# Performance work log

Hardware: AMD Instinct MI355X
Metric: run time of the kernel (lower is better)

The kernel has to match this reference:

```python
import jax, jax.numpy as jnp
import numpy as np

B, T, N, D = 8, 12, 1024, 64
E, M, L = 64, 16, 2


def _ln(x, g, b, eps=1e-5):
    mu = x.mean(-1, keepdims=True)
    var = ((x - mu) ** 2).mean(-1, keepdims=True)
    return (x - mu) * jax.lax.rsqrt(var + eps) * g + b


def setup_inputs() -> dict:
    key = jax.random.key(0)
    ks = jax.random.split(key, 10)
    return {
        "H_temp": jax.random.normal(ks[0], (B, T, N, D), dtype=jnp.float32),
        "A_static": jax.random.uniform(ks[1], (N, N), dtype=jnp.float32),
        "W_Q": jax.random.normal(ks[2], (E, D)) / np.sqrt(D),
        "W_K": jax.random.normal(ks[3], (E, E)) / np.sqrt(E),
        "W_V": jax.random.normal(ks[4], (D, E)) / np.sqrt(E),
        "PHI_m": jax.random.normal(ks[5], (M, E)) / np.sqrt(E),
        "out_W": jax.random.normal(ks[6], (D, D)) / np.sqrt(D),
        "out_b": jnp.zeros((D,)),
        "sma_g": jnp.ones((D,)),
        "sma_b": jnp.zeros((D,)),
        "beta": jnp.asarray(0.5, dtype=jnp.float32),
        "proj_W": jax.random.normal(ks[7], (D, D * (L + 1))) / np.sqrt(D * (L + 1)),
        "proj_b": jnp.zeros((D,)),
        "agg_g": jnp.ones((D,)),
        "agg_b": jnp.zeros((D,)),
    }


def reference(H_temp, A_static, W_Q, W_K, W_V, PHI_m, out_W, out_b,
              sma_g, sma_b, beta, proj_W, proj_b, agg_g, agg_b):
    d = H_temp.shape[-1]
    e = W_Q.shape[0]
    # ---- SpatialMemoryAttention (linear attention with memory slots) ----
    K = PHI_m @ W_K.T                      # [M,E]
    V = PHI_m @ W_V.T                      # [M,d]
    phi_K = jax.nn.elu(K) + 1.0
    KtV = jnp.einsum('me,md->ed', phi_K, V)            # [E,d]
    Q = jnp.einsum('btnd,ed->btne', H_temp, W_Q)       # [B,T,N,E]
    phi_Q = jax.nn.elu(Q) + 1.0
    QK = jnp.einsum('btne,me->btnm', phi_Q, phi_K) / np.sqrt(e)
    A_dyn_qm = jax.nn.softmax(QK, axis=-1)             # [B,T,N,M]
    main_att = jnp.einsum('btne,ed->btnd', phi_Q, KtV)
    mem_val = jnp.einsum('btnm,md->btnd', A_dyn_qm, V)
    Hp = main_att + H_temp
    Hp = jnp.einsum('btnd,od->btno', Hp, out_W) + out_b
    H_prime = _ln(Hp, sma_g, sma_b)                    # [B,T,N,d]
    mv = mem_val.mean(axis=1)                          # [B,N,d]
    A_dynamic = jax.nn.softmax(
        jnp.einsum('bnd,bmd->bnm', mv, mv) / np.sqrt(d), axis=-1)  # [B,N,N]
    # ---- fuse static + dynamic adjacency ----
    deg = A_static.sum(-1) + 1e-12
    dinv = deg ** -0.5
    A_hat = dinv[:, None] * A_static * dinv[None, :]
    bta = jnp.clip(beta, 0.0, 1.0)
    A_fused = bta * A_dynamic + (1.0 - bta) * A_hat[None]
    # ---- L-hop diffusion aggregation (conv1d k=1 == linear) ----
    diffs = [H_prime]
    Xk = H_prime
    for _ in range(L):
        Xk = jnp.einsum('bnm,btmd->btnd', A_fused, Xk)
        diffs.append(Xk)
    cat = jnp.concatenate(diffs, axis=-1)              # [B,T,N,(L+1)d]
    out = jnp.einsum('btnc,oc->btno', cat, proj_W) + proj_b
    H_spatial = _ln(out, agg_g, agg_b)
    return (H_spatial, A_dynamic, A_fused)
```

## Files before the change

kernel.cpp:

```cpp
#include <hip/hip_runtime.h>
#include <math.h>

#define B_ 8
#define T_ 12
#define N_ 1024
#define D_ 64
#define E_ 64
#define M_ 16
#define BT_ (B_*T_)
#define ROWS_ (B_*T_*N_)
#define PAD 68
#define DPAD 72

typedef __attribute__((ext_vector_type(8))) __bf16 bf16x8;
typedef __attribute__((ext_vector_type(4))) __bf16 bf16x4;
typedef __attribute__((ext_vector_type(4))) float f32x4;

__device__ __forceinline__ float elu1(float x) {
    return x > 0.0f ? x + 1.0f : __expf(x);
}


__device__ __forceinline__ void stageT(const float* __restrict__ src, int stride,
                                       float* __restrict__ lds, int tid) {
#pragma unroll
    for (int i = 0; i < 16; ++i) {
        int idx = tid + i * 256;
        int r = idx >> 6, c = idx & 63;
        lds[c * PAD + r] = src[r * stride + c];
    }
}

__device__ __forceinline__ void stageN(const float* __restrict__ src, int stride,
                                       float* __restrict__ lds, int tid) {
#pragma unroll
    for (int i = 0; i < 16; ++i) {
        int idx = tid + i * 256;
        int r = idx >> 6, c = idx & 63;
        lds[r * PAD + c] = src[r * stride + c];
    }
}

__device__ __forceinline__ void mac64(const float* __restrict__ AsT, const float* __restrict__ Bs,
                                      float acc[4][4], int ty, int tx) {
#pragma unroll 8
    for (int k = 0; k < 64; ++k) {
        float4 a = *(const float4*)(AsT + k * PAD + ty * 4);
        float4 b = *(const float4*)(Bs + k * PAD + tx * 4);
        float av[4] = {a.x, a.y, a.z, a.w};
        float bv[4] = {b.x, b.y, b.z, b.w};
#pragma unroll
        for (int i = 0; i < 4; ++i)
#pragma unroll
            for (int j = 0; j < 4; ++j)
                acc[i][j] = fmaf(av[i], bv[j], acc[i][j]);
    }
}

__global__ void k_precompute(const float* __restrict__ PHI, const float* __restrict__ WK,
                             const float* __restrict__ WV, float* __restrict__ phiK,
                             float* __restrict__ Vm, float* __restrict__ KtV) {
    __shared__ float sPhiK[M_ * E_];
    __shared__ float sV[M_ * D_];
    int tid = threadIdx.x;
    for (int i = tid; i < M_ * E_; i += 256) {
        int m = i >> 6, e = i & 63;
        float kk = 0.f, vv = 0.f;
        for (int j = 0; j < E_; ++j) {
            float p = PHI[m * E_ + j];
            kk += p * WK[e * E_ + j];
            vv += p * WV[e * E_ + j];
        }
        float pk = elu1(kk);
        sPhiK[i] = pk; phiK[i] = pk;
        sV[i] = vv;    Vm[i] = vv;
    }
    __syncthreads();
    for (int i = tid; i < E_ * D_; i += 256) {
        int e = i >> 6, d = i & 63;
        float acc = 0.f;
        for (int m = 0; m < M_; ++m) acc += sPhiK[m * E_ + e] * sV[m * D_ + d];
        KtV[i] = acc;
    }
}

__global__ void k_dinv(const float* __restrict__ A, float* __restrict__ dinv) {
    int row = blockIdx.x;
    int tid = threadIdx.x;
    float s = 0.f;
    for (int i = tid; i < N_; i += 256) s += A[(size_t)row * N_ + i];
    for (int off = 32; off; off >>= 1) s += __shfl_xor(s, off, 64);
    __shared__ float red[4];
    if ((tid & 63) == 0) red[tid >> 6] = s;
    __syncthreads();
    if (tid == 0) dinv[row] = rsqrtf(red[0] + red[1] + red[2] + red[3] + 1e-12f);
}

__global__ void k_phiq(const float* __restrict__ H, const float* __restrict__ WQ,
                       float* __restrict__ out) {
    __shared__ __align__(16) float AsT[64 * PAD];
    __shared__ __align__(16) float Bs[64 * PAD];
    int tid = threadIdx.x;
    const float* Arow = H + (size_t)blockIdx.x * 4096;
    stageT(Arow, 64, AsT, tid);
    stageT(WQ, 64, Bs, tid);
    __syncthreads();
    int ty = tid >> 4, tx = tid & 15;
    float acc[4][4] = {};
    mac64(AsT, Bs, acc, ty, tx);
    float* orow = out + (size_t)blockIdx.x * 4096;
#pragma unroll
    for (int i = 0; i < 4; ++i) {
        float4 o;
        o.x = elu1(acc[i][0]); o.y = elu1(acc[i][1]);
        o.z = elu1(acc[i][2]); o.w = elu1(acc[i][3]);
        *(float4*)(orow + (size_t)(ty * 4 + i) * 64 + tx * 4) = o;
    }
}

__global__ void k_attn_mem(const float* __restrict__ phiQ, const float* __restrict__ phiK,
                           const float* __restrict__ Vm, __bf16* __restrict__ mv) {
    __shared__ float pkT[E_ * 17];
    __shared__ float sV[M_ * D_];
    __shared__ float pq[4][D_];
    __shared__ float sa[4][M_];
    int tid = threadIdx.x;
    for (int i = tid; i < M_ * E_; i += 256) {
        int m = i >> 6, e = i & 63;
        pkT[e * 17 + m] = phiK[m * E_ + e];
    }
    for (int i = tid; i < M_ * D_; i += 256) sV[i] = Vm[i];
    __syncthreads();
    int w = tid >> 6, lane = tid & 63;
    int b = blockIdx.x >> 8;
    int n = (blockIdx.x & 255) * 4 + w;
    int m = lane & 15, c = lane >> 4;
    float mvacc = 0.f;
    for (int t = 0; t < T_; ++t) {
        size_t rowoff = ((size_t)(b * T_ + t) * N_ + n) * 64;
        pq[w][lane] = phiQ[rowoff + lane];
        __syncthreads();
        float s = 0.f;
#pragma unroll
        for (int i = 0; i < 16; ++i) {
            int e = c * 16 + i;
            s += pq[w][e] * pkT[e * 17 + m];
        }
        s += __shfl_xor(s, 16, 64);
        s += __shfl_xor(s, 32, 64);
        s *= 0.125f;
        float mx = s;
        mx = fmaxf(mx, __shfl_xor(mx, 1, 64)); mx = fmaxf(mx, __shfl_xor(mx, 2, 64));
        mx = fmaxf(mx, __shfl_xor(mx, 4, 64)); mx = fmaxf(mx, __shfl_xor(mx, 8, 64));
        float ex = __expf(s - mx);
        float sum = ex;
        sum += __shfl_xor(sum, 1, 64); sum += __shfl_xor(sum, 2, 64);
        sum += __shfl_xor(sum, 4, 64); sum += __shfl_xor(sum, 8, 64);
        float a = ex / sum;
        if (lane < 16) sa[w][lane] = a;
        __syncthreads();
        float mval = 0.f;
#pragma unroll
        for (int mm = 0; mm < 16; ++mm) mval += sa[w][mm] * sV[mm * D_ + lane];
        mvacc += mval;
        __syncthreads();
    }
    mv[((size_t)b * N_ + n) * 64 + lane] = (__bf16)(mvacc * (1.0f / 12.0f));
}

__global__ void k_matt(float* __restrict__ buf, const float* __restrict__ KtV,
                       const float* __restrict__ H) {
    __shared__ __align__(16) float AsT[64 * PAD];
    __shared__ __align__(16) float Bs[64 * PAD];
    int tid = threadIdx.x;
    float* rows = buf + (size_t)blockIdx.x * 4096;
    stageT(rows, 64, AsT, tid);
    stageN(KtV, 64, Bs, tid);
    __syncthreads();
    int ty = tid >> 4, tx = tid & 15;
    float acc[4][4] = {};
    mac64(AsT, Bs, acc, ty, tx);
    const float* hrow = H + (size_t)blockIdx.x * 4096;
#pragma unroll
    for (int i = 0; i < 4; ++i) {
        float4 h = *(const float4*)(hrow + (size_t)(ty * 4 + i) * 64 + tx * 4);
        float4 o;
        o.x = acc[i][0] + h.x; o.y = acc[i][1] + h.y;
        o.z = acc[i][2] + h.z; o.w = acc[i][3] + h.w;
        *(float4*)(rows + (size_t)(ty * 4 + i) * 64 + tx * 4) = o;
    }
}

__global__ void k_outln(const float* __restrict__ buf, const float* __restrict__ outW,
                        const float* __restrict__ outb, const float* __restrict__ g,
                        const float* __restrict__ bb, __bf16* __restrict__ Hn,
                        __bf16* __restrict__ Ht) {
    __shared__ __align__(16) float AsT[64 * PAD];
    __shared__ __align__(16) float Bs[64 * PAD];
    int tid = threadIdx.x;
    const float* rows = buf + (size_t)blockIdx.x * 4096;
    stageT(rows, 64, AsT, tid);
    stageT(outW, 64, Bs, tid);
    __syncthreads();
    int ty = tid >> 4, tx = tid & 15;
    float acc[4][4] = {};
    mac64(AsT, Bs, acc, ty, tx);
    __syncthreads();
    __bf16* Cs = (__bf16*)Bs;
    float gg[4], bbv[4], bi[4];
#pragma unroll
    for (int j = 0; j < 4; ++j) {
        int o = tx * 4 + j;
        gg[j] = g[o]; bbv[j] = bb[o]; bi[j] = outb[o];
    }
    size_t base = (size_t)blockIdx.x * 4096;
#pragma unroll
    for (int i = 0; i < 4; ++i) {
        float v[4];
#pragma unroll
        for (int j = 0; j < 4; ++j) v[j] = acc[i][j] + bi[j];
        float s = v[0] + v[1] + v[2] + v[3];
        s += __shfl_xor(s, 1, 64); s += __shfl_xor(s, 2, 64);
        s += __shfl_xor(s, 4, 64); s += __shfl_xor(s, 8, 64);
        float mu = s * (1.0f / 64.0f);
        float qv = 0.f;
#pragma unroll
        for (int j = 0; j < 4; ++j) { float d = v[j] - mu; qv += d * d; }
        qv += __shfl_xor(qv, 1, 64); qv += __shfl_xor(qv, 2, 64);
        qv += __shfl_xor(qv, 4, 64); qv += __shfl_xor(qv, 8, 64);
        float rstd = rsqrtf(qv * (1.0f / 64.0f) + 1e-5f);
        int row = ty * 4 + i;
        bf16x4 ob;
#pragma unroll
        for (int j = 0; j < 4; ++j) {
            float o = (v[j] - mu) * rstd * gg[j] + bbv[j];
            ob[j] = (__bf16)o;
            Cs[row * DPAD + tx * 4 + j] = (__bf16)o;
        }
        *(bf16x4*)(Hn + base + (size_t)row * 64 + tx * 4) = ob;
    }
    __syncthreads();
    int bt = blockIdx.x >> 4;
    int n0 = (blockIdx.x & 15) * 64;
    size_t tbase = (size_t)bt * 64 * N_;
#pragma unroll
    for (int i = 0; i < 2; ++i) {
        int d = (tid >> 3) + i * 32;
        int n8 = (tid & 7) * 8;
        bf16x8 v;
#pragma unroll
        for (int j = 0; j < 8; ++j) {
            int jj = (j + tid) & 7;
            v[jj] = Cs[(n8 + jj) * DPAD + d];
        }
        *(bf16x8*)(Ht + tbase + (size_t)d * N_ + n0 + n8) = v;
    }
}

__global__ void k_adyn_mfma(const __bf16* __restrict__ mvb_all, const float* __restrict__ Ast,
                            const float* __restrict__ dinv, const float* __restrict__ beta,
                            float* __restrict__ Adyn, float* __restrict__ Afu,
                            __bf16* __restrict__ Afb) {
    __shared__ __align__(16) __bf16 As[16 * DPAD];
    __shared__ __align__(16) __bf16 Bs[256 * DPAD];
    __shared__ float redm[4][16];
    __shared__ float reds[4][16];
    int tid = threadIdx.x;
    int b = blockIdx.x >> 6, n0 = (blockIdx.x & 63) * 16;
    const __bf16* mvb = mvb_all + (size_t)b * N_ * 64;
    {
        int r = tid >> 4, c4 = (tid & 15) * 4;
        *(bf16x4*)&As[r * DPAD + c4] = *(const bf16x4*)(mvb + (size_t)(n0 + r) * 64 + c4);
    }
    int w = tid >> 6, lane = tid & 63, q = lane >> 4, lr = lane & 15;
    f32x4 acc[4][4];
#pragma unroll
    for (int c = 0; c < 4; ++c)
#pragma unroll
        for (int tj = 0; tj < 4; ++tj) acc[c][tj] = (f32x4)(0.0f);
    int brow = tid >> 3, bcol = (tid & 7) * 8;
    for (int c = 0; c < 4; ++c) {
        __syncthreads();
#pragma unroll
        for (int i = 0; i < 8; ++i) {
            int r = brow + i * 32;
            *(bf16x8*)&Bs[r * DPAD + bcol] = *(const bf16x8*)(mvb + (size_t)(c * 256 + r) * 64 + bcol);
        }
        __syncthreads();
#pragma unroll
// ... 56 lines not shown
    float inv[4];
#pragma unroll
    for (int rr = 0; rr < 4; ++rr) {
        int row = q * 4 + rr;
        inv[rr] = 1.0f / (reds[0][row] + reds[1][row] + reds[2][row] + reds[3][row]);
    }
    float bta = fminf(fmaxf(beta[0], 0.0f), 1.0f);
    float omb = 1.0f - bta;
    float dc[4][4];
#pragma unroll
    for (int c = 0; c < 4; ++c)
#pragma unroll
        for (int tj = 0; tj < 4; ++tj) dc[c][tj] = dinv[c * 256 + w * 64 + tj * 16 + lr];
#pragma unroll
    for (int rr = 0; rr < 4; ++rr) {
        int n = n0 + q * 4 + rr;
        float dn = omb * dinv[n];
        size_t ro = ((size_t)b * N_ + n) * N_;
        const float* arow = Ast + (size_t)n * N_;
#pragma unroll
        for (int c = 0; c < 4; ++c)
#pragma unroll
            for (int tj = 0; tj < 4; ++tj) {
                int col = c * 256 + w * 64 + tj * 16 + lr;
                float p = acc[c][tj][rr] * inv[rr];
                float fu = bta * p + dn * arow[col] * dc[c][tj];
                Adyn[ro + col] = p;
                Afu[ro + col] = fu;
                Afb[ro + col] = (__bf16)fu;
            }
    }
}

__global__ void k_diffuse_mfma(const __bf16* __restrict__ Afb, const __bf16* __restrict__ Xt,
                               __bf16* __restrict__ Xn_out, __bf16* __restrict__ Xt_out) {
    __shared__ __align__(16) __bf16 As[128 * DPAD];
    __shared__ __align__(16) __bf16 Bs[64 * DPAD];
    int tid = threadIdx.x;
    int bt = blockIdx.y, b = bt / T_;
    int n0 = blockIdx.x * 128;
    const __bf16* A = Afb + (size_t)b * N_ * N_ + (size_t)n0 * N_;
    const __bf16* X = Xt + (size_t)bt * 64 * N_;
    int w = tid >> 6, lane = tid & 63, q = lane >> 4, lr = lane & 15;
    int mw = w * 32;
    f32x4 acc[2][4];
#pragma unroll
    for (int i = 0; i < 2; ++i)
#pragma unroll
        for (int j = 0; j < 4; ++j) acc[i][j] = (f32x4)(0.0f);
    int arow = tid >> 3, acol = (tid & 7) * 8;
    for (int kc = 0; kc < 16; ++kc) {
        if (kc) __syncthreads();
#pragma unroll
        for (int i = 0; i < 4; ++i) {
            int r = arow + i * 32;
            *(bf16x8*)&As[r * DPAD + acol] = *(const bf16x8*)(A + (size_t)r * N_ + kc * 64 + acol);
        }
#pragma unroll
        for (int i = 0; i < 2; ++i) {
            int r = arow + i * 32;
            *(bf16x8*)&Bs[r * DPAD + acol] = *(const bf16x8*)(X + (size_t)r * N_ + kc * 64 + acol);
        }
        __syncthreads();
#pragma unroll
        for (int ks = 0; ks < 2; ++ks) {
            int kb = ks * 32 + q * 8;
            bf16x8 a0 = *(const bf16x8*)&As[(mw + lr) * DPAD + kb];
            bf16x8 a1 = *(const bf16x8*)&As[(mw + 16 + lr) * DPAD + kb];
#pragma unroll
            for (int tj = 0; tj < 4; ++tj) {
                bf16x8 bf = *(const bf16x8*)&Bs[(tj * 16 + lr) * DPAD + kb];
                acc[0][tj] = __builtin_amdgcn_mfma_f32_16x16x32_bf16(a0, bf, acc[0][tj], 0, 0, 0);
                acc[1][tj] = __builtin_amdgcn_mfma_f32_16x16x32_bf16(a1, bf, acc[1][tj], 0, 0, 0);
            }
        }
    }
    __syncthreads();
    __bf16* Cs = As;
#pragma unroll
    for (int ti = 0; ti < 2; ++ti)
#pragma unroll
        for (int tj = 0; tj < 4; ++tj)
#pragma unroll
            for (int r = 0; r < 4; ++r)
                Cs[(mw + ti * 16 + q * 4 + r) * DPAD + tj * 16 + lr] = (__bf16)acc[ti][tj][r];
    __syncthreads();
    size_t obase = (size_t)bt * N_ * 64;
#pragma unroll
    for (int i = 0; i < 4; ++i) {
        int r = arow + i * 32;
        *(bf16x8*)(Xn_out + obase + (size_t)(n0 + r) * 64 + acol) = *(const bf16x8*)&Cs[r * DPAD + acol];
    }
    if (Xt_out) {
        size_t tbase = (size_t)bt * 64 * N_;
#pragma unroll
        for (int i = 0; i < 4; ++i) {
            int d = (tid >> 4) + i * 16;
            int n8 = (tid & 15) * 8;
            bf16x8 v;
#pragma unroll
            for (int j = 0; j < 8; ++j) {
                int jj = (j + tid) & 7;
                v[jj] = Cs[(n8 + jj) * DPAD + d];
            }
            *(bf16x8*)(Xt_out + tbase + (size_t)d * N_ + n0 + n8) = v;
        }
    }
}

__global__ void k_projln_mfma(const __bf16* __restrict__ Hn, const __bf16* __restrict__ X1n,
                              const __bf16* __restrict__ X2n, const float* __restrict__ PW,
                              const float* __restrict__ pb, const float* __restrict__ g,
                              const float* __restrict__ bb, float* __restrict__ out) {
    __shared__ __align__(16) __bf16 As[128 * DPAD];
    __shared__ __align__(16) __bf16 Bs[64 * DPAD];
    int tid = threadIdx.x;
    size_t r0 = (size_t)blockIdx.x * 128;
    int w = tid >> 6, lane = tid & 63, q = lane >> 4, lr = lane & 15;
    int mw = w * 32;
    f32x4 acc[2][4];
#pragma unroll
    for (int i = 0; i < 2; ++i)
#pragma unroll
        for (int j = 0; j < 4; ++j) acc[i][j] = (f32x4)(0.0f);
    const __bf16* srcs[3] = {Hn, X1n, X2n};
    int arow = tid >> 3, acol = (tid & 7) * 8;
    int prow = tid >> 2, pc16 = (tid & 3) * 16;
    for (int c = 0; c < 3; ++c) {
        if (c) __syncthreads();
        const __bf16* S = srcs[c] + r0 * 64;
#pragma unroll
        for (int i = 0; i < 4; ++i) {
            int r = arow + i * 32;
            *(bf16x8*)&As[r * DPAD + acol] = *(const bf16x8*)(S + (size_t)r * 64 + acol);
        }
        const float* P = PW + (size_t)prow * 192 + c * 64 + pc16;
        float4 f0 = *(const float4*)(P + 0);
        float4 f1 = *(const float4*)(P + 4);
        float4 f2 = *(const float4*)(P + 8);
        float4 f3 = *(const float4*)(P + 12);
        bf16x8 w0, w1;
        w0[0] = (__bf16)f0.x; w0[1] = (__bf16)f0.y; w0[2] = (__bf16)f0.z; w0[3] = (__bf16)f0.w;
        w0[4] = (__bf16)f1.x; w0[5] = (__bf16)f1.y; w0[6] = (__bf16)f1.z; w0[7] = (__bf16)f1.w;
        w1[0] = (__bf16)f2.x; w1[1] = (__bf16)f2.y; w1[2] = (__bf16)f2.z; w1[3] = (__bf16)f2.w;
        w1[4] = (__bf16)f3.x; w1[5] = (__bf16)f3.y; w1[6] = (__bf16)f3.z; w1[7] = (__bf16)f3.w;
        *(bf16x8*)&Bs[prow * DPAD + pc16] = w0;
        *(bf16x8*)&Bs[prow * DPAD + pc16 + 8] = w1;
        __syncthreads();
#pragma unroll
        for (int ks = 0; ks < 2; ++ks) {
            int kb = ks * 32 + q * 8;
            bf16x8 a0 = *(const bf16x8*)&As[(mw + lr) * DPAD + kb];
            bf16x8 a1 = *(const bf16x8*)&As[(mw + 16 + lr) * DPAD + kb];
#pragma unroll
            for (int tj = 0; tj < 4; ++tj) {
                bf16x8 bf = *(const bf16x8*)&Bs[(tj * 16 + lr) * DPAD + kb];
                acc[0][tj] = __builtin_amdgcn_mfma_f32_16x16x32_bf16(a0, bf, acc[0][tj], 0, 0, 0);
                acc[1][tj] = __builtin_amdgcn_mfma_f32_16x16x32_bf16(a1, bf, acc[1][tj], 0, 0, 0);
            }
        }
    }
    float pbv[4], gv[4], bv2[4];
#pragma unroll
    for (int tj = 0; tj < 4; ++tj) {
        int col = tj * 16 + lr;
        pbv[tj] = pb[col]; gv[tj] = g[col]; bv2[tj] = bb[col];
    }
#pragma unroll
    for (int ti = 0; ti < 2; ++ti) {
#pragma unroll
        for (int r = 0; r < 4; ++r) {
            float v[4];
            float s = 0.f;
#pragma unroll
            for (int tj = 0; tj < 4; ++tj) { v[tj] = acc[ti][tj][r] + pbv[tj]; s += v[tj]; }
            s += __shfl_xor(s, 1, 64); s += __shfl_xor(s, 2, 64);
            s += __shfl_xor(s, 4, 64); s += __shfl_xor(s, 8, 64);
            float mu = s * (1.0f / 64.0f);
            float qv = 0.f;
#pragma unroll
            for (int tj = 0; tj < 4; ++tj) { float d = v[tj] - mu; qv += d * d; }
            qv += __shfl_xor(qv, 1, 64); qv += __shfl_xor(qv, 2, 64);
            qv += __shfl_xor(qv, 4, 64); qv += __shfl_xor(qv, 8, 64);
            float rstd = rsqrtf(qv * (1.0f / 64.0f) + 1e-5f);
            size_t row = r0 + mw + ti * 16 + q * 4 + r;
#pragma unroll
            for (int tj = 0; tj < 4; ++tj)
                out[row * 64 + tj * 16 + lr] = (v[tj] - mu) * rstd * gv[tj] + bv2[tj];
        }
    }
}

extern "C" void kernel_launch(void* const* d_in, const int* in_sizes, int n_in,
                              void* d_out, int out_size, void* d_ws, size_t ws_size,
                              hipStream_t stream) {
    const float* H    = (const float*)d_in[0];
    const float* Ast  = (const float*)d_in[1];
    const float* WQ   = (const float*)d_in[2];
    const float* WK   = (const float*)d_in[3];
    const float* WV   = (const float*)d_in[4];
    const float* PHI  = (const float*)d_in[5];
    const float* outW = (const float*)d_in[6];
    const float* outb = (const float*)d_in[7];
    const float* smag = (const float*)d_in[8];
    const float* smab = (const float*)d_in[9];
    const float* beta = (const float*)d_in[10];
    const float* PW   = (const float*)d_in[11];
    const float* pb   = (const float*)d_in[12];
    const float* aggg = (const float*)d_in[13];
    const float* aggb = (const float*)d_in[14];

    float* out  = (float*)d_out;
    float* Hsp  = out;
    float* Adyn = out + (size_t)ROWS_ * 64;
    float* Afu  = Adyn + (size_t)B_ * N_ * N_;

    float* ws   = (float*)d_ws;
    float* BUF0 = ws;
    float* phiK = ws + (size_t)ROWS_ * 64;
    float* Vm   = phiK + M_ * E_;
    float* KtV  = Vm + M_ * D_;
    float* dinv = KtV + E_ * D_;
    __bf16* mvb = (__bf16*)(dinv + N_);
    __bf16* Hn  = mvb + (size_t)B_ * N_ * 64;
    __bf16* Ht  = Hn + (size_t)ROWS_ * 64;
    __bf16* Afb = Ht + (size_t)ROWS_ * 64;
    __bf16* X1n = (__bf16*)BUF0;
    __bf16* X1t = X1n + (size_t)ROWS_ * 64;
    __bf16* X2n = Ht;

    k_precompute<<<1, 256, 0, stream>>>(PHI, WK, WV, phiK, Vm, KtV);
    k_dinv<<<N_, 256, 0, stream>>>(Ast, dinv);
    k_phiq<<<ROWS_ / 64, 256, 0, stream>>>(H, WQ, BUF0);
    k_attn_mem<<<B_ * N_ / 4, 256, 0, stream>>>(BUF0, phiK, Vm, mvb);
    k_matt<<<ROWS_ / 64, 256, 0, stream>>>(BUF0, KtV, H);
    k_outln<<<ROWS_ / 64, 256, 0, stream>>>(BUF0, outW, outb, smag, smab, Hn, Ht);
    k_adyn_mfma<<<B_ * N_ / 16, 256, 0, stream>>>(mvb, Ast, dinv, beta, Adyn, Afu, Afb);
    k_diffuse_mfma<<<dim3(8, BT_), 256, 0, stream>>>(Afb, Ht, X1n, X1t);
    k_diffuse_mfma<<<dim3(8, BT_), 256, 0, stream>>>(Afb, X1t, X2n, (__bf16*)nullptr);
    k_projln_mfma<<<ROWS_ / 128, 256, 0, stream>>>(Hn, X1n, X2n, PW, pb, aggg, aggb, Hsp);
}
```

Baseline: 320.4 us.

## Fuse attention spine into one MFMA kernel and fold projection into second diffusion

Replaces the four scalar-FMA spine kernels (phiQ, memory attention, main attention, output+LN) with a single bf16 MFMA kernel that keeps intermediates in LDS. A separate small kernel reduces per-timestep memory values over T. The second diffusion hop is fused with the final projection+LayerNorm so X2 is never written to global memory, and the weights are pre-converted to bf16 once. This removes several full-size fp32 round trips through global memory, at the cost of extra bf16 rounding in the attention path and a larger memval buffer.

```diff
diff --git a/kernel.cpp b/kernel.cpp
--- a/kernel.cpp
+++ b/kernel.cpp
@@ -20,46 +20,12 @@
     return x > 0.0f ? x + 1.0f : __expf(x);
 }
 
-
-__device__ __forceinline__ void stageT(const float* __restrict__ src, int stride,
-                                       float* __restrict__ lds, int tid) {
-#pragma unroll
-    for (int i = 0; i < 16; ++i) {
-        int idx = tid + i * 256;
-        int r = idx >> 6, c = idx & 63;
-        lds[c * PAD + r] = src[r * stride + c];
-    }
-}
-
-__device__ __forceinline__ void stageN(const float* __restrict__ src, int stride,
-                                       float* __restrict__ lds, int tid) {
-#pragma unroll
-    for (int i = 0; i < 16; ++i) {
-        int idx = tid + i * 256;
-        int r = idx >> 6, c = idx & 63;
-        lds[r * PAD + c] = src[r * stride + c];
-    }
-}
-
-__device__ __forceinline__ void mac64(const float* __restrict__ AsT, const float* __restrict__ Bs,
-                                      float acc[4][4], int ty, int tx) {
-#pragma unroll 8
-    for (int k = 0; k < 64; ++k) {
-        float4 a = *(const float4*)(AsT + k * PAD + ty * 4);
-        float4 b = *(const float4*)(Bs + k * PAD + tx * 4);
-        float av[4] = {a.x, a.y, a.z, a.w};
-        float bv[4] = {b.x, b.y, b.z, b.w};
-#pragma unroll
-        for (int i = 0; i < 4; ++i)
-#pragma unroll
-            for (int j = 0; j < 4; ++j)
-                acc[i][j] = fmaf(av[i], bv[j], acc[i][j]);
-    }
-}
-
 __global__ void k_precompute(const float* __restrict__ PHI, const float* __restrict__ WK,
-                             const float* __restrict__ WV, float* __restrict__ phiK,
-                             float* __restrict__ Vm, float* __restrict__ KtV) {
+                             const float* __restrict__ WV, const float* __restrict__ WQ,
+                             const float* __restrict__ outW, const float* __restrict__ PW,
+                             __bf16* __restrict__ phiKb, __bf16* __restrict__ Vtb,
+                             __bf16* __restrict__ KtVtb, __bf16* __restrict__ WQb,
+                             __bf16* __restrict__ outWb, __bf16* __restrict__ PWb) {
     __shared__ float sPhiK[M_ * E_];
     __shared__ float sV[M_ * D_];
     int tid = threadIdx.x;
@@ -72,16 +38,25 @@
             vv += p * WV[e * E_ + j];
         }
         float pk = elu1(kk);
-        sPhiK[i] = pk; phiK[i] = pk;
-        sV[i] = vv;    Vm[i] = vv;
+        sPhiK[i] = pk; phiKb[i] = (__bf16)pk;
+        sV[i] = vv;
     }
     __syncthreads();
-    for (int i = tid; i < E_ * D_; i += 256) {
-        int e = i >> 6, d = i & 63;
+    for (int i = tid; i < 64 * 32; i += 256) {
+        int d = i >> 5, m = i & 31;
+        Vtb[i] = (m < M_) ? (__bf16)sV[m * 64 + d] : (__bf16)0.0f;
+    }
+    for (int i = tid; i < 4096; i += 256) {
+        int d = i >> 6, e = i & 63;
         float acc = 0.f;
-        for (int m = 0; m < M_; ++m) acc += sPhiK[m * E_ + e] * sV[m * D_ + d];
-        KtV[i] = acc;
-    }
+        for (int m = 0; m < M_; ++m) acc += sPhiK[m * 64 + e] * sV[m * 64 + d];
+        KtVtb[i] = (__bf16)acc;
+    }
+    for (int i = tid; i < 4096; i += 256) {
+        WQb[i] = (__bf16)WQ[i];
+        outWb[i] = (__bf16)outW[i];
+    }
+    for (int i = tid; i < 64 * 192; i += 256) PWb[i] = (__bf16)PW[i];
 }
 
 __global__ void k_dinv(const float* __restrict__ A, float* __restrict__ dinv) {
@@ -96,152 +71,165 @@
     if (tid == 0) dinv[row] = rsqrtf(red[0] + red[1] + red[2] + red[3] + 1e-12f);
 }
 
-__global__ void k_phiq(const float* __restrict__ H, const float* __restrict__ WQ,
-                       float* __restrict__ out) {
-    __shared__ __align__(16) float AsT[64 * PAD];
-    __shared__ __align__(16) float Bs[64 * PAD];
+__global__ void k_spine(const float* __restrict__ H, const __bf16* __restrict__ WQb,
+                        const __bf16* __restrict__ phiKb, const __bf16* __restrict__ Vtb,
+                        const __bf16* __restrict__ KtVtb, const __bf16* __restrict__ outWb,
+                        const float* __restrict__ outb, const float* __restrict__ g,
+                        const float* __restrict__ bb, __bf16* __restrict__ memval,
+                        __bf16* __restrict__ Hn, __bf16* __restrict__ Ht) {
+    __shared__ __align__(16) __bf16 As[64 * DPAD];
+    __shared__ __align__(16) __bf16 Ps[64 * DPAD];
+    __shared__ __align__(16) __bf16 Ms[64 * DPAD];
+    __shared__ __align__(16) __bf16 Pp[4][16 * 40];
     int tid = threadIdx.x;
-    const float* Arow = H + (size_t)blockIdx.x * 4096;
-    stageT(Arow, 64, AsT, tid);
-    stageT(WQ, 64, Bs, tid);
+    int w = tid >> 6, lane = tid & 63, q = lane >> 4, lr = lane & 15;
+    int rw = w * 16;
+    const float* Hrow = H + (size_t)blockIdx.x * 4096;
+    {
+        int r = tid >> 2, c0 = (tid & 3) * 16;
+        float4 f0 = *(const float4*)(Hrow + r * 64 + c0);
+        float4 f1 = *(const float4*)(Hrow + r * 64 + c0 + 4);
+        float4 f2 = *(const float4*)(Hrow + r * 64 + c0 + 8);
+        float4 f3 = *(const float4*)(Hrow + r * 64 + c0 + 12);
+        bf16x8 h0, h1;
+        h0[0]=(__bf16)f0.x; h0[1]=(__bf16)f0.y; h0[2]=(__bf16)f0.z; h0[3]=(__bf16)f0.w;
+        h0[4]=(__bf16)f1.x; h0[5]=(__bf16)f1.y; h0[6]=(__bf16)f1.z; h0[7]=(__bf16)f1.w;
+        h1[0]=(__bf16)f2.x; h1[1]=(__bf16)f2.y; h1[2]=(__bf16)f2.z; h1[3]=(__bf16)f2.w;
+        h1[4]=(__bf16)f3.x; h1[5]=(__bf16)f3.y; h1[6]=(__bf16)f3.z; h1[7]=(__bf16)f3.w;
+        *(bf16x8*)&As[r * DPAD + c0] = h0;
+        *(bf16x8*)&As[r * DPAD + c0 + 8] = h1;
+    }
+#pragma unroll
+    for (int i = 0; i < 10; ++i) Pp[w][lane * 10 + i] = (__bf16)0.0f;
     __syncthreads();
-    int ty = tid >> 4, tx = tid & 15;
-    float acc[4][4] = {};
-    mac64(AsT, Bs, acc, ty, tx);
-    float* orow = out + (size_t)blockIdx.x * 4096;
-#pragma unroll
-    for (int i = 0; i < 4; ++i) {
-        float4 o;
-        o.x = elu1(acc[i][0]); o.y = elu1(acc[i][1]);
-        o.z = elu1(acc[i][2]); o.w = elu1(acc[i][3]);
-        *(float4*)(orow + (size_t)(ty * 4 + i) * 64 + tx * 4) = o;
-    }
-}
-
-__global__ void k_attn_mem(const float* __restrict__ phiQ, const float* __restrict__ phiK,
-                           const float* __restrict__ Vm, __bf16* __restrict__ mv) {
-    __shared__ float pkT[E_ * 17];
-    __shared__ float sV[M_ * D_];
-    __shared__ float pq[4][D_];
-    __shared__ float sa[4][M_];
-    int tid = threadIdx.x;
-    for (int i = tid; i < M_ * E_; i += 256) {
-        int m = i >> 6, e = i & 63;
-        pkT[e * 17 + m] = phiK[m * E_ + e];
-    }
-    for (int i = tid; i < M_ * D_; i += 256) sV[i] = Vm[i];
-    __syncthreads();
-    int w = tid >> 6, lane = tid & 63;
-    int b = blockIdx.x >> 8;
-    int n = (blockIdx.x & 255) * 4 + w;
-    int m = lane & 15, c = lane >> 4;
-    float mvacc = 0.f;
-    for (int t = 0; t < T_; ++t) {
-        size_t rowoff = ((size_t)(b * T_ + t) * N_ + n) * 64;
-        pq[w][lane] = phiQ[rowoff + lane];
-        __syncthreads();
-        float s = 0.f;
-#pragma unroll
-        for (int i = 0; i < 16; ++i) {
-            int e = c * 16 + i;
-            s += pq[w][e] * pkT[e * 17 + m];
-        }
-        s += __shfl_xor(s, 16, 64);
-        s += __shfl_xor(s, 32, 64);
-        s *= 0.125f;
+
+    f32x4 qacc[4];
+#pragma unroll
+    for (int tj = 0; tj < 4; ++tj) qacc[tj] = (f32x4)(0.0f);
+#pragma unroll
+    for (int ks = 0; ks < 2; ++ks) {
+        int kb = ks * 32 + q * 8;
+        bf16x8 a = *(const bf16x8*)&As[(rw + lr) * DPAD + kb];
+#pragma unroll
+        for (int tj = 0; tj < 4; ++tj) {
+            bf16x8 bv = *(const bf16x8*)(WQb + (size_t)(tj * 16 + lr) * 64 + kb);
+            qacc[tj] = __builtin_amdgcn_mfma_f32_16x16x32_bf16(a, bv, qacc[tj], 0, 0, 0);
+        }
+    }
+#pragma unroll
+    for (int tj = 0; tj < 4; ++tj)
+#pragma unroll
+        for (int r = 0; r < 4; ++r)
+            Ps[(rw + q * 4 + r) * DPAD + tj * 16 + lr] = (__bf16)elu1(qacc[tj][r]);
+
+    f32x4 sacc = (f32x4)(0.0f);
+#pragma unroll
+    for (int ks = 0; ks < 2; ++ks) {
+        int kb = ks * 32 + q * 8;
+        bf16x8 a = *(const bf16x8*)&Ps[(rw + lr) * DPAD + kb];
+        bf16x8 bv = *(const bf16x8*)(phiKb + (size_t)lr * 64 + kb);
+        sacc = __builtin_amdgcn_mfma_f32_16x16x32_bf16(a, bv, sacc, 0, 0, 0);
+    }
+#pragma unroll
+    for (int r = 0; r < 4; ++r) {
+        float s = sacc[r];
         float mx = s;
         mx = fmaxf(mx, __shfl_xor(mx, 1, 64)); mx = fmaxf(mx, __shfl_xor(mx, 2, 64));
         mx = fmaxf(mx, __shfl_xor(mx, 4, 64)); mx = fmaxf(mx, __shfl_xor(mx, 8, 64));
-        float ex = __expf(s - mx);
-        float sum = ex;
+        float e = __expf(0.125f * (s - mx));
+        float sum = e;
         sum += __shfl_xor(sum, 1, 64); sum += __shfl_xor(sum, 2, 64);
         sum += __shfl_xor(sum, 4, 64); sum += __shfl_xor(sum, 8, 64);
-        float a = ex / sum;
-        if (lane < 16) sa[w][lane] = a;
-        __syncthreads();
-        float mval = 0.f;
-#pragma unroll
-        for (int mm = 0; mm < 16; ++mm) mval += sa[w][mm] * sV[mm * D_ + lane];
-        mvacc += mval;
-        __syncthreads();
-    }
-    mv[((size_t)b * N_ + n) * 64 + lane] = (__bf16)(mvacc * (1.0f / 12.0f));
-}
-
-__global__ void k_matt(float* __restrict__ buf, const float* __restrict__ KtV,
-                       const float* __restrict__ H) {
-    __shared__ __align__(16) float AsT[64 * PAD];
-    __shared__ __align__(16) float Bs[64 * PAD];
-    int tid = threadIdx.x;
-    float* rows = buf + (size_t)blockIdx.x * 4096;
-    stageT(rows, 64, AsT, tid);
-    stageN(KtV, 64, Bs, tid);
-    __syncthreads();
-    int ty = tid >> 4, tx = tid & 15;
-    float acc[4][4] = {};
-    mac64(AsT, Bs, acc, ty, tx);
-    const float* hrow = H + (size_t)blockIdx.x * 4096;
-#pragma unroll
-    for (int i = 0; i < 4; ++i) {
-        float4 h = *(const float4*)(hrow + (size_t)(ty * 4 + i) * 64 + tx * 4);
-        float4 o;
-        o.x = acc[i][0] + h.x; o.y = acc[i][1] + h.y;
-        o.z = acc[i][2] + h.z; o.w = acc[i][3] + h.w;
-        *(float4*)(rows + (size_t)(ty * 4 + i) * 64 + tx * 4) = o;
-    }
-}
-
-__global__ void k_outln(const float* __restrict__ buf, const float* __restrict__ outW,
-                        const float* __restrict__ outb, const float* __restrict__ g,
-                        const float* __restrict__ bb, __bf16* __restrict__ Hn,
-                        __bf16* __restrict__ Ht) {
-    __shared__ __align__(16) float AsT[64 * PAD];
-    __shared__ __align__(16) float Bs[64 * PAD];
-    int tid = threadIdx.x;
-    const float* rows = buf + (size_t)blockIdx.x * 4096;
-    stageT(rows, 64, AsT, tid);
-    stageT(outW, 64, Bs, tid);
-    __syncthreads();
-    int ty = tid >> 4, tx = tid & 15;
-    float acc[4][4] = {};
-    mac64(AsT, Bs, acc, ty, tx);
-    __syncthreads();
-    __bf16* Cs = (__bf16*)Bs;
-    float gg[4], bbv[4], bi[4];
-#pragma unroll
-    for (int j = 0; j < 4; ++j) {
-        int o = tx * 4 + j;
-        gg[j] = g[o]; bbv[j] = bb[o]; bi[j] = outb[o];
-    }
-    size_t base = (size_t)blockIdx.x * 4096;
-#pragma unroll
-    for (int i = 0; i < 4; ++i) {
+        Pp[w][(q * 4 + r) * 40 + lr] = (__bf16)(e / sum);
+    }
+    f32x4 macc[4];
+#pragma unroll
+    for (int tj = 0; tj < 4; ++tj) macc[tj] = (f32x4)(0.0f);
+    {
+        bf16x8 ap = *(const bf16x8*)&Pp[w][lr * 40 + q * 8];
+#pragma unroll
+        for (int tj = 0; tj < 4; ++tj) {
+            bf16x8 bv = *(const bf16x8*)(Vtb + (size_t)(tj * 16 + lr) * 32 + q * 8);
+            macc[tj] = __builtin_amdgcn_mfma_f32_16x16x32_bf16(ap, bv, macc[tj], 0, 0, 0);
+        }
+    }
+#pragma unroll
+    for (int tj = 0; tj < 4; ++tj)
+#pragma unroll
+        for (int r = 0; r < 4; ++r)
+            Ms[(rw + q * 4 + r) * DPAD + tj * 16 + lr] = (__bf16)macc[tj][r];
+
+    f32x4 aacc[4];
+#pragma unroll
+    for (int tj = 0; tj < 4; ++tj) aacc[tj] = (f32x4)(0.0f);
+#pragma unroll
+    for (int ks = 0; ks < 2; ++ks) {
+        int kb = ks * 32 + q * 8;
+        bf16x8 a = *(const bf16x8*)&Ps[(rw + lr) * DPAD + kb];
+#pragma unroll
+        for (int tj = 0; tj < 4; ++tj) {
+            bf16x8 bv = *(const bf16x8*)(KtVtb + (size_t)(tj * 16 + lr) * 64 + kb);
+            aacc[tj] = __builtin_amdgcn_mfma_f32_16x16x32_bf16(a, bv, aacc[tj], 0, 0, 0);
+        }
+    }
+#pragma unroll
+    for (int tj = 0; tj < 4; ++tj)
+#pragma unroll
+        for (int r = 0; r < 4; ++r) {
+            float hp = aacc[tj][r] + Hrow[(rw + q * 4 + r) * 64 + tj * 16 + lr];
+            As[(rw + q * 4 + r) * DPAD + tj * 16 + lr] = (__bf16)hp;
+        }
+
+    f32x4 oacc[4];
+#pragma unroll
+    for (int tj = 0; tj < 4; ++tj) oacc[tj] = (f32x4)(0.0f);
+#pragma unroll
+    for (int ks = 0; ks < 2; ++ks) {
+        int kb = ks * 32 + q * 8;
+        bf16x8 a = *(const bf16x8*)&As[(rw + lr) * DPAD + kb];
+#pragma unroll
+        for (int tj = 0; tj < 4; ++tj) {
+            bf16x8 bv = *(const bf16x8*)(outWb + (size_t)(tj * 16 + lr) * 64 + kb);
+            oacc[tj] = __builtin_amdgcn_mfma_f32_16x16x32_bf16(a, bv, oacc[tj], 0, 0, 0);
+        }
+    }
+    float biasv[4], gv[4], bv2[4];
+#pragma unroll
+    for (int tj = 0; tj < 4; ++tj) {
+        int col = tj * 16 + lr;
+        biasv[tj] = outb[col]; gv[tj] = g[col]; bv2[tj] = bb[col];
+    }
+#pragma unroll
+    for (int r = 0; r < 4; ++r) {
         float v[4];
-#pragma unroll
-        for (int j = 0; j < 4; ++j) v[j] = acc[i][j] + bi[j];
-        float s = v[0] + v[1] + v[2] + v[3];
+        float s = 0.f;
+#pragma unroll
+        for (int tj = 0; tj < 4; ++tj) { v[tj] = oacc[tj][r] + biasv[tj]; s += v[tj]; }
         s += __shfl_xor(s, 1, 64); s += __shfl_xor(s, 2, 64);
         s += __shfl_xor(s, 4, 64); s += __shfl_xor(s, 8, 64);
         float mu = s * (1.0f / 64.0f);
         float qv = 0.f;
 #pragma unroll
-        for (int j = 0; j < 4; ++j) { float d = v[j] - mu; qv += d * d; }
+        for (int tj = 0; tj < 4; ++tj) { float d = v[tj] - mu; qv += d * d; }
         qv += __shfl_xor(qv, 1, 64); qv += __shfl_xor(qv, 2, 64);
         qv += __shfl_xor(qv, 4, 64); qv += __shfl_xor(qv, 8, 64);
         float rstd = rsqrtf(qv * (1.0f / 64.0f) + 1e-5f);
-        int row = ty * 4 + i;
-        bf16x4 ob;
-#pragma unroll
-        for (int j = 0; j < 4; ++j) {
-            float o = (v[j] - mu) * rstd * gg[j] + bbv[j];
-            ob[j] = (__bf16)o;
-            Cs[row * DPAD + tx * 4 + j] = (__bf16)o;
-        }
-        *(bf16x4*)(Hn + base + (size_t)row * 64 + tx * 4) = ob;
+#pragma unroll
+        for (int tj = 0; tj < 4; ++tj)
+            Ps[(rw + q * 4 + r) * DPAD + tj * 16 + lr] =
+                (__bf16)((v[tj] - mu) * rstd * gv[tj] + bv2[tj]);
     }
     __syncthreads();
-    int bt = blockIdx.x >> 4;
-    int n0 = (blockIdx.x & 15) * 64;
+
+    size_t base = (size_t)blockIdx.x * 4096;
+    {
+        int r = tid >> 2, c0 = (tid & 3) * 16;
+        *(bf16x8*)(memval + base + (size_t)r * 64 + c0)     = *(const bf16x8*)&Ms[r * DPAD + c0];
+        *(bf16x8*)(memval + base + (size_t)r * 64 + c0 + 8) = *(const bf16x8*)&Ms[r * DPAD + c0 + 8];
+        *(bf16x8*)(Hn + base + (size_t)r * 64 + c0)         = *(const bf16x8*)&Ps[r * DPAD + c0];
+        *(bf16x8*)(Hn + base + (size_t)r * 64 + c0 + 8)     = *(const bf16x8*)&Ps[r * DPAD + c0 + 8];
+    }
+    int bt = blockIdx.x >> 4, n0b = (blockIdx.x & 15) * 64;
     size_t tbase = (size_t)bt * 64 * N_;
 #pragma unroll
     for (int i = 0; i < 2; ++i) {
@@ -251,10 +239,27 @@
 #pragma unroll
         for (int j = 0; j < 8; ++j) {
             int jj = (j + tid) & 7;
-            v[jj] = Cs[(n8 + jj) * DPAD + d];
-        }
-        *(bf16x8*)(Ht + tbase + (size_t)d * N_ + n0 + n8) = v;
-    }
+            v[jj] = Ps[(n8 + jj) * DPAD + d];
+        }
+        *(bf16x8*)(Ht + tbase + (size_t)d * N_ + n0b + n8) = v;
+    }
+}
+
+__global__ void k_mvred(const __bf16* __restrict__ memval, __bf16* __restrict__ mvb) {
+    int idx = (blockIdx.x * 256 + threadIdx.x) * 4;
+    int b = idx >> 16;
+    int off = idx & 65535;
+    const __bf16* p = memval + (size_t)b * T_ * 65536 + off;
+    float a0 = 0.f, a1 = 0.f, a2 = 0.f, a3 = 0.f;
+#pragma unroll
+    for (int t = 0; t < T_; ++t) {
+        bf16x4 v = *(const bf16x4*)(p + (size_t)t * 65536);
+        a0 += (float)v[0]; a1 += (float)v[1]; a2 += (float)v[2]; a3 += (float)v[3];
+    }
+    bf16x4 o;
+    o[0] = (__bf16)(a0 * (1.0f / 12.0f)); o[1] = (__bf16)(a1 * (1.0f / 12.0f));
+    o[2] = (__bf16)(a2 * (1.0f / 12.0f)); o[3] = (__bf16)(a3 * (1.0f / 12.0f));
+    *(bf16x4*)(mvb + idx) = o;
 }
 
 __global__ void k_adyn_mfma(const __bf16* __restrict__ mvb_all, const float* __restrict__ Ast,
@@ -377,51 +382,45 @@
     }
 }
 
-__global__ void k_diffuse_mfma(const __bf16* __restrict__ Afb, const __bf16* __restrict__ Xt,
-                               __bf16* __restrict__ Xn_out, __bf16* __restrict__ Xt_out) {
-    __shared__ __align__(16) __bf16 As[128 * DPAD];
-    __shared__ __align__(16) __bf16 Bs[64 * DPAD];
+__global__ void k_diffuse1(const __bf16* __restrict__ Afb, const __bf16* __restrict__ Xt,
+                           __bf16* __restrict__ Xn_out, __bf16* __restrict__ Xt_out) {
+    __shared__ __align__(16) __bf16 Cs[128 * DPAD];
     int tid = threadIdx.x;
     int bt = blockIdx.y, b = bt / T_;
     int n0 = blockIdx.x * 128;
+    int w = tid >> 6, lane = tid & 63, q = lane >> 4, lr = lane & 15;
+    int mw = w * 32;
     const __bf16* A = Afb + (size_t)b * N_ * N_ + (size_t)n0 * N_;
     const __bf16* X = Xt + (size_t)bt * 64 * N_;
-    int w = tid >> 6, lane = tid & 63, q = lane >> 4, lr = lane & 15;
-    int mw = w * 32;
+    const __bf16* a0p = A + (size_t)(mw + lr) * N_ + q * 8;
+    const __bf16* a1p = A + (size_t)(mw + 16 + lr) * N_ + q * 8;
+    const __bf16* b0p = X + (size_t)(lr) * N_ + q * 8;
+    const __bf16* b1p = X + (size_t)(16 + lr) * N_ + q * 8;
+    const __bf16* b2p = X + (size_t)(32 + lr) * N_ + q * 8;
+    const __bf16* b3p = X + (size_t)(48 + lr) * N_ + q * 8;
     f32x4 acc[2][4];
 #pragma unroll
     for (int i = 0; i < 2; ++i)
 #pragma unroll
         for (int j = 0; j < 4; ++j) acc[i][j] = (f32x4)(0.0f);
-    int arow = tid >> 3, acol = (tid & 7) * 8;
-    for (int kc = 0; kc < 16; ++kc) {
-        if (kc) __syncthreads();
-#pragma unroll
-        for (int i = 0; i < 4; ++i) {
-            int r = arow + i * 32;
-            *(bf16x8*)&As[r * DPAD + acol] = *(const bf16x8*)(A + (size_t)r * N_ + kc * 64 + acol);
-        }
-#pragma unroll
-        for (int i = 0; i < 2; ++i) {
-            int r = arow + i * 32;
-            *(bf16x8*)&Bs[r * DPAD + acol] = *(const bf16x8*)(X + (size_t)r * N_ + kc * 64 + acol);
-        }
-        __syncthreads();
-#pragma unroll
-        for (int ks = 0; ks < 2; ++ks) {
-            int kb = ks * 32 + q * 8;
-            bf16x8 a0 = *(const bf16x8*)&As[(mw + lr) * DPAD + kb];
-            bf16x8 a1 = *(const bf16x8*)&As[(mw + 16 + lr) * DPAD + kb];
-#pragma unroll
-            for (int tj = 0; tj < 4; ++tj) {
-                bf16x8 bf = *(const bf16x8*)&Bs[(tj * 16 + lr) * DPAD + kb];
-                acc[0][tj] = __builtin_amdgcn_mfma_f32_16x16x32_bf16(a0, bf, acc[0][tj], 0, 0, 0);
-                acc[1][tj] = __builtin_amdgcn_mfma_f32_16x16x32_bf16(a1, bf, acc[1][tj], 0, 0, 0);
-            }
-        }
-    }
-    __syncthreads();
-    __bf16* Cs = As;
+#pragma unroll 8
+    for (int kk = 0; kk < 32; ++kk) {
+        int k = kk * 32;
+        bf16x8 a0 = *(const bf16x8*)(a0p + k);
+        bf16x8 a1 = *(const bf16x8*)(a1p + k);
+        bf16x8 b0 = *(const bf16x8*)(b0p + k);
+        bf16x8 b1 = *(const bf16x8*)(b1p + k);
+        bf16x8 b2 = *(const bf16x8*)(b2p + k);
+        bf16x8 b3 = *(const bf16x8*)(b3p + k);
+        acc[0][0] = __builtin_amdgcn_mfma_f32_16x16x32_bf16(a0, b0, acc[0][0], 0, 0, 0);
+        acc[1][0] = __builtin_amdgcn_mfma_f32_16x16x32_bf16(a1, b0, acc[1][0], 0, 0, 0);
+        acc[0][1] = __builtin_amdgcn_mfma_f32_16x16x32_bf16(a0, b1, acc[0][1], 0, 0, 0);
+        acc[1][1] = __builtin_amdgcn_mfma_f32_16x16x32_bf16(a1, b1, acc[1][1], 0, 0, 0);
+        acc[0][2] = __builtin_amdgcn_mfma_f32_16x16x32_bf16(a0, b2, acc[0][2], 0, 0, 0);
+        acc[1][2] = __builtin_amdgcn_mfma_f32_16x16x32_bf16(a1, b2, acc[1][2], 0, 0, 0);
+        acc[0][3] = __builtin_amdgcn_mfma_f32_16x16x32_bf16(a0, b3, acc[0][3], 0, 0, 0);
+        acc[1][3] = __builtin_amdgcn_mfma_f32_16x16x32_bf16(a1, b3, acc[1][3], 0, 0, 0);
+    }
 #pragma unroll
     for (int ti = 0; ti < 2; ++ti)
 #pragma unroll
@@ -430,79 +429,109 @@
             for (int r = 0; r < 4; ++r)
                 Cs[(mw + ti * 16 + q * 4 + r) * DPAD + tj * 16 + lr] = (__bf16)acc[ti][tj][r];
     __syncthreads();
-    size_t obase = (size_t)bt * N_ * 64;
+    size_t obase = (size_t)bt * N_ * 64 + (size_t)n0 * 64;
+#pragma unroll
+    for (int i = 0; i < 2; ++i) {
+        int r = (tid >> 2) + i * 64, c0 = (tid & 3) * 16;
+        *(bf16x8*)(Xn_out + obase + (size_t)r * 64 + c0)     = *(const bf16x8*)&Cs[r * DPAD + c0];
+        *(bf16x8*)(Xn_out + obase + (size_t)r * 64 + c0 + 8) = *(const bf16x8*)&Cs[r * DPAD + c0 + 8];
+    }
+    size_t tbase = (size_t)bt * 64 * N_;
 #pragma unroll
     for (int i = 0; i < 4; ++i) {
-        int r = arow + i * 32;
-        *(bf16x8*)(Xn_out + obase + (size_t)(n0 + r) * 64 + acol) = *(const bf16x8*)&Cs[r * DPAD + acol];
-    }
-    if (Xt_out) {
-        size_t tbase = (size_t)bt * 64 * N_;
-#pragma unroll
-        for (int i = 0; i < 4; ++i) {
-            int d = (tid >> 4) + i * 16;
-            int n8 = (tid & 15) * 8;
-            bf16x8 v;
-#pragma unroll
-            for (int j = 0; j < 8; ++j) {
-                int jj = (j + tid) & 7;
-                v[jj] = Cs[(n8 + jj) * DPAD + d];
-            }
-            *(bf16x8*)(Xt_out + tbase + (size_t)d * N_ + n0 + n8) = v;
-        }
-    }
-}
-
-__global__ void k_projln_mfma(const __bf16* __restrict__ Hn, const __bf16* __restrict__ X1n,
-                              const __bf16* __restrict__ X2n, const float* __restrict__ PW,
-                              const float* __restrict__ pb, const float* __restrict__ g,
-                              const float* __restrict__ bb, float* __restrict__ out) {
-    __shared__ __align__(16) __bf16 As[128 * DPAD];
-    __shared__ __align__(16) __bf16 Bs[64 * DPAD];
+        int d = (tid >> 4) + i * 16;
+        int n8 = (tid & 15) * 8;
+        bf16x8 v;
+#pragma unroll
+        for (int j = 0; j < 8; ++j) {
+            int jj = (j + tid) & 7;
+            v[jj] = Cs[(n8 + jj) * DPAD + d];
+        }
+        *(bf16x8*)(Xt_out + tbase + (size_t)d * N_ + n0 + n8) = v;
+    }
+}
+
+__global__ void k_diffuse2_proj(const __bf16* __restrict__ Afb, const __bf16* __restrict__ X1t,
+                                const __bf16* __restrict__ Hn, const __bf16* __restrict__ X1n,
+                                const __bf16* __restrict__ PWb, const float* __restrict__ pb,
+                                const float* __restrict__ g, const float* __restrict__ bb,
+                                float* __restrict__ out) {
+    __shared__ __align__(16) __bf16 Cs[128 * DPAD];
     int tid = threadIdx.x;
-    size_t r0 = (size_t)blockIdx.x * 128;
+    int bt = blockIdx.y, b = bt / T_;
+    int n0 = blockIdx.x * 128;
     int w = tid >> 6, lane = tid & 63, q = lane >> 4, lr = lane & 15;
     int mw = w * 32;
+    const __bf16* A = Afb + (size_t)b * N_ * N_ + (size_t)n0 * N_;
+    const __bf16* X = X1t + (size_t)bt * 64 * N_;
+    const __bf16* a0p = A + (size_t)(mw + lr) * N_ + q * 8;
+    const __bf16* a1p = A + (size_t)(mw + 16 + lr) * N_ + q * 8;
+    const __bf16* b0p = X + (size_t)(lr) * N_ + q * 8;
+    const __bf16* b1p = X + (size_t)(16 + lr) * N_ + q * 8;
+    const __bf16* b2p = X + (size_t)(32 + lr) * N_ + q * 8;
+    const __bf16* b3p = X + (size_t)(48 + lr) * N_ + q * 8;
     f32x4 acc[2][4];
 #pragma unroll
     for (int i = 0; i < 2; ++i)
 #pragma unroll
         for (int j = 0; j < 4; ++j) acc[i][j] = (f32x4)(0.0f);
-    const __bf16* srcs[3] = {Hn, X1n, X2n};
-    int arow = tid >> 3, acol = (tid & 7) * 8;
-    int prow = tid >> 2, pc16 = (tid & 3) * 16;
-    for (int c = 0; c < 3; ++c) {
-        if (c) __syncthreads();
-        const __bf16* S = srcs[c] + r0 * 64;
-#pragma unroll
-        for (int i = 0; i < 4; ++i) {
-            int r = arow + i * 32;
-            *(bf16x8*)&As[r * DPAD + acol] = *(const bf16x8*)(S + (size_t)r * 64 + acol);
-        }
-        const float* P = PW + (size_t)prow * 192 + c * 64 + pc16;
-        float4 f0 = *(const float4*)(P + 0);
-        float4 f1 = *(const float4*)(P + 4);
-        float4 f2 = *(const float4*)(P + 8);
-        float4 f3 = *(const float4*)(P + 12);
-        bf16x8 w0, w1;
-        w0[0] = (__bf16)f0.x; w0[1] = (__bf16)f0.y; w0[2] = (__bf16)f0.z; w0[3] = (__bf16)f0.w;
-        w0[4] = (__bf16)f1.x; w0[5] = (__bf16)f1.y; w0[6] = (__bf16)f1.z; w0[7] = (__bf16)f1.w;
-        w1[0] = (__bf16)f2.x; w1[1] = (__bf16)f2.y; w1[2] = (__bf16)f2.z; w1[3] = (__bf16)f2.w;
-        w1[4] = (__bf16)f3.x; w1[5] = (__bf16)f3.y; w1[6] = (__bf16)f3.z; w1[7] = (__bf16)f3.w;
-        *(bf16x8*)&Bs[prow * DPAD + pc16] = w0;
-        *(bf16x8*)&Bs[prow * DPAD + pc16 + 8] = w1;
-        __syncthreads();
+#pragma unroll 8
+    for (int kk = 0; kk < 32; ++kk) {
+        int k = kk * 32;
+        bf16x8 a0 = *(const bf16x8*)(a0p + k);
+        bf16x8 a1 = *(const bf16x8*)(a1p + k);
+        bf16x8 b0 = *(const bf16x8*)(b0p + k);
+        bf16x8 b1 = *(const bf16x8*)(b1p + k);
+        bf16x8 b2 = *(const bf16x8*)(b2p + k);
+        bf16x8 b3 = *(const bf16x8*)(b3p + k);
+        acc[0][0] = __builtin_amdgcn_mfma_f32_16x16x32_bf16(a0, b0, acc[0][0], 0, 0, 0);
+        acc[1][0] = __builtin_amdgcn_mfma_f32_16x16x32_bf16(a1, b0, acc[1][0], 0, 0, 0);
+        acc[0][1] = __builtin_amdgcn_mfma_f32_16x16x32_bf16(a0, b1, acc[0][1], 0, 0, 0);
+        acc[1][1] = __builtin_amdgcn_mfma_f32_16x16x32_bf16(a1, b1, acc[1][1], 0, 0, 0);
+        acc[0][2] = __builtin_amdgcn_mfma_f32_16x16x32_bf16(a0, b2, acc[0][2], 0, 0, 0);
+        acc[1][2] = __builtin_amdgcn_mfma_f32_16x16x32_bf16(a1, b2, acc[1][2], 0, 0, 0);
+        acc[0][3] = __builtin_amdgcn_mfma_f32_16x16x32_bf16(a0, b3, acc[0][3], 0, 0, 0);
+        acc[1][3] = __builtin_amdgcn_mfma_f32_16x16x32_bf16(a1, b3, acc[1][3], 0, 0, 0);
+    }
+#pragma unroll
+    for (int ti = 0; ti < 2; ++ti)
+#pragma unroll
+        for (int tj = 0; tj < 4; ++tj)
+#pragma unroll
+            for (int r = 0; r < 4; ++r)
+                Cs[(mw + ti * 16 + q * 4 + r) * DPAD + tj * 16 + lr] = (__bf16)acc[ti][tj][r];
+    f32x4 pacc[2][4];
+#pragma unroll
+    for (int i = 0; i < 2; ++i)
+#pragma unroll
+        for (int j = 0; j < 4; ++j) pacc[i][j] = (f32x4)(0.0f);
+    size_t row0 = (size_t)bt * N_ + n0;
+#pragma unroll
+    for (int c = 0; c < 2; ++c) {
+        const __bf16* S = (c ? X1n : Hn) + row0 * 64;
 #pragma unroll
         for (int ks = 0; ks < 2; ++ks) {
             int kb = ks * 32 + q * 8;
-            bf16x8 a0 = *(const bf16x8*)&As[(mw + lr) * DPAD + kb];
-            bf16x8 a1 = *(const bf16x8*)&As[(mw + 16 + lr) * DPAD + kb];
+            bf16x8 a0 = *(const bf16x8*)(S + (size_t)(mw + lr) * 64 + kb);
+            bf16x8 a1 = *(const bf16x8*)(S + (size_t)(mw + 16 + lr) * 64 + kb);
 #pragma unroll
             for (int tj = 0; tj < 4; ++tj) {
-                bf16x8 bf = *(const bf16x8*)&Bs[(tj * 16 + lr) * DPAD + kb];
-                acc[0][tj] = __builtin_amdgcn_mfma_f32_16x16x32_bf16(a0, bf, acc[0][tj], 0, 0, 0);
-                acc[1][tj] = __builtin_amdgcn_mfma_f32_16x16x32_bf16(a1, bf, acc[1][tj], 0, 0, 0);
+                bf16x8 bv = *(const bf16x8*)(PWb + (size_t)(tj * 16 + lr) * 192 + c * 64 + kb);
+                pacc[0][tj] = __builtin_amdgcn_mfma_f32_16x16x32_bf16(a0, bv, pacc[0][tj], 0, 0, 0);
+                pacc[1][tj] = __builtin_amdgcn_mfma_f32_16x16x32_bf16(a1, bv, pacc[1][tj], 0, 0, 0);
             }
+        }
+    }
+#pragma unroll
+    for (int ks = 0; ks < 2; ++ks) {
+        int kb = ks * 32 + q * 8;
+        bf16x8 a0 = *(const bf16x8*)&Cs[(mw + lr) * DPAD + kb];
+        bf16x8 a1 = *(const bf16x8*)&Cs[(mw + 16 + lr) * DPAD + kb];
+#pragma unroll
+        for (int tj = 0; tj < 4; ++tj) {
+            bf16x8 bv = *(const bf16x8*)(PWb + (size_t)(tj * 16 + lr) * 192 + 128 + kb);
+            pacc[0][tj] = __builtin_amdgcn_mfma_f32_16x16x32_bf16(a0, bv, pacc[0][tj], 0, 0, 0);
+            pacc[1][tj] = __builtin_amdgcn_mfma_f32_16x16x32_bf16(a1, bv, pacc[1][tj], 0, 0, 0);
         }
     }
     float pbv[4], gv[4], bv2[4];
@@ -518,7 +547,7 @@
             float v[4];
             float s = 0.f;
 #pragma unroll
-            for (int tj = 0; tj < 4; ++tj) { v[tj] = acc[ti][tj][r] + pbv[tj]; s += v[tj]; }
+            for (int tj = 0; tj < 4; ++tj) { v[tj] = pacc[ti][tj][r] + pbv[tj]; s += v[tj]; }
             s += __shfl_xor(s, 1, 64); s += __shfl_xor(s, 2, 64);
             s += __shfl_xor(s, 4, 64); s += __shfl_xor(s, 8, 64);
             float mu = s * (1.0f / 64.0f);
@@ -528,7 +557,7 @@
             qv += __shfl_xor(qv, 1, 64); qv += __shfl_xor(qv, 2, 64);
             qv += __shfl_xor(qv, 4, 64); qv += __shfl_xor(qv, 8, 64);
             float rstd = rsqrtf(qv * (1.0f / 64.0f) + 1e-5f);
-            size_t row = r0 + mw + ti * 16 + q * 4 + r;
+            size_t row = row0 + mw + ti * 16 + q * 4 + r;
 #pragma unroll
             for (int tj = 0; tj < 4; ++tj)
                 out[row * 64 + tj * 16 + lr] = (v[tj] - mu) * rstd * gv[tj] + bv2[tj];
@@ -560,28 +589,29 @@
     float* Adyn = out + (size_t)ROWS_ * 64;
     float* Afu  = Adyn + (size_t)B_ * N_ * N_;
 
-    float* ws   = (float*)d_ws;
-    float* BUF0 = ws;
-    float* phiK = ws + (size_t)ROWS_ * 64;
-    float* Vm   = phiK + M_ * E_;
-    float* KtV  = Vm + M_ * D_;
-    float* dinv = KtV + E_ * D_;
-    __bf16* mvb = (__bf16*)(dinv + N_);
-    __bf16* Hn  = mvb + (size_t)B_ * N_ * 64;
-    __bf16* Ht  = Hn + (size_t)ROWS_ * 64;
-    __bf16* Afb = Ht + (size_t)ROWS_ * 64;
-    __bf16* X1n = (__bf16*)BUF0;
-    __bf16* X1t = X1n + (size_t)ROWS_ * 64;
-    __bf16* X2n = Ht;
-
-    k_precompute<<<1, 256, 0, stream>>>(PHI, WK, WV, phiK, Vm, KtV);
+    __bf16* memval = (__bf16*)d_ws;
+    __bf16* Hn   = memval + (size_t)ROWS_ * 64;
+    __bf16* Ht   = Hn + (size_t)ROWS_ * 64;
+    __bf16* X1n  = Ht + (size_t)ROWS_ * 64;
+    __bf16* X1t  = X1n + (size_t)ROWS_ * 64;
+    __bf16* Afb  = X1t + (size_t)ROWS_ * 64;
+    __bf16* mvb  = Afb + (size_t)B_ * N_ * N_;
+    __bf16* phiKb = mvb + (size_t)B_ * N_ * 64;
+    __bf16* Vtb   = phiKb + M_ * E_;
+    __bf16* KtVtb = Vtb + 64 * 32;
+    __bf16* WQb   = KtVtb + 4096;
+    __bf16* outWb = WQb + 4096;
+    __bf16* PWb   = outWb + 4096;
+    float*  dinv  = (float*)(PWb + 64 * 192);
+
+    k_precompute<<<1, 256, 0, stream>>>(PHI, WK, WV, WQ, outW, PW,
+                                        phiKb, Vtb, KtVtb, WQb, outWb, PWb);
     k_dinv<<<N_, 256, 0, stream>>>(Ast, dinv);
-    k_phiq<<<ROWS_ / 64, 256, 0, stream>>>(H, WQ, BUF0);
-    k_attn_mem<<<B_ * N_ / 4, 256, 0, stream>>>(BUF0, phiK, Vm, mvb);
-    k_matt<<<ROWS_ / 64, 256, 0, stream>>>(BUF0, KtV, H);
-    k_outln<<<ROWS_ / 64, 256, 0, stream>>>(BUF0, outW, outb, smag, smab, Hn, Ht);
+    k_spine<<<ROWS_ / 64, 256, 0, stream>>>(H, WQb, phiKb, Vtb, KtVtb, outWb,
+                                            outb, smag, smab, memval, Hn, Ht);
+    k_mvred<<<(B_ * N_ * 64 / 4) / 256, 256, 0, stream>>>(memval, mvb);
     k_adyn_mfma<<<B_ * N_ / 16, 256, 0, stream>>>(mvb, Ast, dinv, beta, Adyn, Afu, Afb);
-    k_diffuse_mfma<<<dim3(8, BT_), 256, 0, stream>>>(Afb, Ht, X1n, X1t);
-    k_diffuse_mfma<<<dim3(8, BT_), 256, 0, stream>>>(Afb, X1t, X2n, (__bf16*)nullptr);
-    k_projln_mfma<<<ROWS_ / 128, 256, 0, stream>>>(Hn, X1n, X2n, PW, pb, aggg, aggb, Hsp);
-}
+    k_diffuse1<<<dim3(8, BT_), 256, 0, stream>>>(Afb, Ht, X1n, X1t);
+    k_diffuse2_proj<<<dim3(8, BT_), 256, 0, stream>>>(Afb, X1t, Hn, X1n, PWb,
+                                                      pb, aggg, aggb, Hsp);
+}
```

Result: slower. 367.7 us (+14.8%).
